# Optimization experiments

Hardware: AMD Instinct MI355X
Metric: run time of the kernel (lower is better)

## Reference

```python
import jax, jax.numpy as jnp
import numpy as np
from jax.ops import segment_sum

N_NODES = 100000


def _add_self_loops(edge_index, n):
    loop = jnp.arange(n, dtype=edge_index.dtype)
    src = jnp.concatenate([edge_index[0], loop])
    dst = jnp.concatenate([edge_index[1], loop])
    return src, dst


def _gcn_conv(x, W, b, src, dst, n):
    # PyG GCNConv: h = X W; out[i] = sum_j norm(j,i) h[j] + b, with self-loops
    h = x @ W                                             # [N, out]
    deg = segment_sum(jnp.ones_like(src, dtype=x.dtype), dst, num_segments=n)
    dinv = jnp.where(deg > 0, jax.lax.rsqrt(deg), 0.0)    # deg^{-1/2}
    norm = dinv[src] * dinv[dst]                          # [E]
    msg = h[src] * norm[:, None]                          # gather + scale
    out = segment_sum(msg, dst, num_segments=n)           # scatter-add
    return out + b


def setup_inputs() -> dict:
    key = jax.random.key(0)
    ks = jax.random.split(key, 8)
    x = jax.random.normal(ks[0], (N_NODES, 128), dtype=jnp.float32)
    edge_index = jax.random.randint(ks[1], (2, 600000), 0, N_NODES, dtype=jnp.int64)
    s1 = 1.0 / np.sqrt(128); s2 = 1.0 / np.sqrt(64); s3 = 1.0 / np.sqrt(32)
    return {
        "x": x,
        "edge_index": edge_index,
        "W1": jax.random.uniform(ks[2], (128, 64), jnp.float32, -s1, s1),
        "b1": jnp.zeros((64,), jnp.float32),
        "W2": jax.random.uniform(ks[3], (64, 32), jnp.float32, -s2, s2),
        "b2": jnp.zeros((32,), jnp.float32),
        "Wc": jax.random.uniform(ks[4], (32, 1), jnp.float32, -s3, s3),
        "bc": jnp.zeros((1,), jnp.float32),
    }


def reference(x, edge_index, W1, b1, W2, b2, Wc, bc):
    n = x.shape[0]
    src, dst = _add_self_loops(edge_index, n)
    h = jax.nn.relu(_gcn_conv(x, W1, b1, src, dst, n))
    h = jax.nn.relu(_gcn_conv(h, W2, b2, src, dst, n))
    return h @ Wc + bc
```

## Files before the change

kernel.cpp:

```cpp
#include <hip/hip_runtime.h>


#define SCAN_THREADS 256
#define SCAN_PER_T   8
#define SCAN_TILE    (SCAN_THREADS * SCAN_PER_T)

__global__ __launch_bounds__(256) void count_kernel(const int* __restrict__ dst,
                                                    int* __restrict__ deg, int E) {
    int e = blockIdx.x * blockDim.x + threadIdx.x;
    if (e < E) atomicAdd(&deg[dst[e]], 1);
}

__global__ __launch_bounds__(SCAN_THREADS) void tile_reduce_kernel(const int* __restrict__ deg,
                                                                   int* __restrict__ bsum,
                                                                   int n) {
    __shared__ int s[SCAN_THREADS];
    int t = threadIdx.x;
    int gbase = blockIdx.x * SCAN_TILE + t * SCAN_PER_T;
    int local = 0;
#pragma unroll
    for (int k = 0; k < SCAN_PER_T; ++k) {
        int i = gbase + k;
        if (i < n) local += deg[i];
    }
    s[t] = local;
    __syncthreads();
    for (int off = SCAN_THREADS / 2; off > 0; off >>= 1) {
        if (t < off) s[t] += s[t + off];
        __syncthreads();
    }
    if (t == 0) bsum[blockIdx.x] = s[0];
}

__global__ __launch_bounds__(SCAN_THREADS) void scan_bsums_kernel(int* __restrict__ bsum,
                                                                  int* __restrict__ row_ptr,
                                                                  int nb, int n) {
    __shared__ int s[SCAN_THREADS];
    int t = threadIdx.x;
    s[t] = (t < nb) ? bsum[t] : 0;
    __syncthreads();
    for (int off = 1; off < SCAN_THREADS; off <<= 1) {
        int v = (t >= off) ? s[t - off] : 0;
        __syncthreads();
        s[t] += v;
        __syncthreads();
    }
    if (t < nb) bsum[t] = (t == 0) ? 0 : s[t - 1];
    if (t == 0) row_ptr[n] = s[nb - 1];
}

__global__ __launch_bounds__(SCAN_THREADS) void tile_apply_kernel(int* __restrict__ deg,
                                                                  const int* __restrict__ bsum,
                                                                  int* __restrict__ row_ptr,
                                                                  float* __restrict__ dinv,
                                                                  int n) {
    __shared__ int s[SCAN_THREADS];
    int t = threadIdx.x;
    int gbase = blockIdx.x * SCAN_TILE + t * SCAN_PER_T;

    int d[SCAN_PER_T];
    int inc[SCAN_PER_T];
    int run = 0;
#pragma unroll
    for (int k = 0; k < SCAN_PER_T; ++k) {
        int i = gbase + k;
        d[k] = (i < n) ? deg[i] : 0;
        run += d[k];
        inc[k] = run;
    }
    s[t] = run;
    __syncthreads();
    for (int off = 1; off < SCAN_THREADS; off <<= 1) {
        int v = (t >= off) ? s[t - off] : 0;
        __syncthreads();
        s[t] += v;
        __syncthreads();
    }
    int base = bsum[blockIdx.x] + ((t == 0) ? 0 : s[t - 1]);
#pragma unroll
    for (int k = 0; k < SCAN_PER_T; ++k) {
        int i = gbase + k;
        if (i < n) {
            int ex = base + inc[k] - d[k];
            row_ptr[i] = ex;
            deg[i] = ex;
            dinv[i] = rsqrtf((float)(d[k] + 1));
        }
    }
}

__global__ __launch_bounds__(256) void fill_kernel(const int* __restrict__ src,
                                                   const int* __restrict__ dst,
                                                   int* __restrict__ cursor,
                                                   int* __restrict__ col, int E) {
    int e = blockIdx.x * blockDim.x + threadIdx.x;
    if (e < E) {
        int pos = atomicAdd(&cursor[dst[e]], 1);
        col[pos] = src[e];
    }
}

template <int IN, int OUT, int BM, int TM, int TN>
__global__ __launch_bounds__(256) void gemm_tiled(const float* __restrict__ X,
                                                  const float* __restrict__ W,
                                                  float* __restrict__ H, int n) {
    constexpr int BK = 32;
    constexpr int XST = BK + 1;
    constexpr int NTX = OUT / TN;
    constexpr int NF4 = BM * BK / 4;
    static_assert(NTX * (BM / TM) == 256, "thread mapping");

    __shared__ float Ws[IN * OUT];
    __shared__ float Xs[BM * XST];

    const int t = threadIdx.x;
    for (int i = t; i < IN * OUT / 4; i += 256)
        ((float4*)Ws)[i] = ((const float4*)W)[i];

    const int node0 = blockIdx.x * BM;
    const int tx = t % NTX;
    const int ty = t / NTX;
    const int row0 = ty * TM;
    const int jb = tx * TN;

    float acc[TM][TN];
#pragma unroll
    for (int i = 0; i < TM; ++i)
#pragma unroll
        for (int j = 0; j < TN; ++j) acc[i][j] = 0.f;

    for (int kt = 0; kt < IN / BK; ++kt) {
        __syncthreads();
        for (int f = t; f < NF4; f += 256) {
            int nd = f >> 3;
            int kq = f & 7;
            float4 val = make_float4(0.f, 0.f, 0.f, 0.f);
            if (node0 + nd < n)
                val = *(const float4*)(X + (size_t)(node0 + nd) * IN + kt * BK + kq * 4);
            float* p = Xs + nd * XST + kq * 4;
            p[0] = val.x; p[1] = val.y; p[2] = val.z; p[3] = val.w;
        }
        __syncthreads();

#pragma unroll 4
        for (int k = 0; k < BK; ++k) {
            float xv[TM];
#pragma unroll
            for (int i = 0; i < TM; ++i) xv[i] = Xs[(row0 + i) * XST + k];
            float4 wv = *(const float4*)(Ws + (size_t)(kt * BK + k) * OUT + jb);
#pragma unroll
            for (int i = 0; i < TM; ++i) {
                acc[i][0] += xv[i] * wv.x;
                acc[i][1] += xv[i] * wv.y;
                acc[i][2] += xv[i] * wv.z;
                acc[i][3] += xv[i] * wv.w;
            }
        }
    }

#pragma unroll
    for (int i = 0; i < TM; ++i) {
        int node = node0 + row0 + i;
        if (node < n)
            *(float4*)(H + (size_t)node * OUT + jb) =
                make_float4(acc[i][0], acc[i][1], acc[i][2], acc[i][3]);
    }
}

template <int F>
__global__ __launch_bounds__(256) void agg_relu_kernel(const int* __restrict__ row_ptr,
                                                       const int* __restrict__ col,
                                                       const float* __restrict__ dinv,
                                                       const float* __restrict__ H,
                                                       const float* __restrict__ b,
                                                       float* __restrict__ OUT, int n) {
    constexpr int TPE = F / 4;
    int t = blockIdx.x * blockDim.x + threadIdx.x;
    int node = t / TPE;
    int c = t % TPE;
    if (node >= n) return;
    int rs = row_ptr[node], re = row_ptr[node + 1];
    float di = dinv[node];
    float4 acc = make_float4(0.f, 0.f, 0.f, 0.f);
    int e = rs;
    for (; e + 1 < re; e += 2) {
        int s0 = col[e], s1 = col[e + 1];
        float w0 = dinv[s0], w1 = dinv[s1];
        float4 v0 = *(const float4*)(H + (size_t)s0 * F + c * 4);
        float4 v1 = *(const float4*)(H + (size_t)s1 * F + c * 4);
        acc.x += w0 * v0.x + w1 * v1.x;
        acc.y += w0 * v0.y + w1 * v1.y;
        acc.z += w0 * v0.z + w1 * v1.z;
        acc.w += w0 * v0.w + w1 * v1.w;
    }
    if (e < re) {
        int s0 = col[e];
        float w0 = dinv[s0];
        float4 v0 = *(const float4*)(H + (size_t)s0 * F + c * 4);
        acc.x += w0 * v0.x; acc.y += w0 * v0.y;
        acc.z += w0 * v0.z; acc.w += w0 * v0.w;
    }
    float4 hs = *(const float4*)(H + (size_t)node * F + c * 4);
    float4 bb = *(const float4*)(b + c * 4);
    float d2 = di * di;
    float4 r;
    r.x = di * acc.x + d2 * hs.x + bb.x;
    r.y = di * acc.y + d2 * hs.y + bb.y;
    r.z = di * acc.z + d2 * hs.z + bb.z;
    r.w = di * acc.w + d2 * hs.w + bb.w;
    r.x = r.x > 0.f ? r.x : 0.f;
    r.y = r.y > 0.f ? r.y : 0.f;
    r.z = r.z > 0.f ? r.z : 0.f;
    r.w = r.w > 0.f ? r.w : 0.f;
    *(float4*)(OUT + (size_t)node * F + c * 4) = r;
}

__global__ __launch_bounds__(256) void agg_final_kernel(const int* __restrict__ row_ptr,
                                                        const int* __restrict__ col,
                                                        const float* __restrict__ dinv,
                                                        const float* __restrict__ H,
                                                        const float* __restrict__ b2,
                                                        const float* __restrict__ Wc,
                                                        const float* __restrict__ bc,
                                                        float* __restrict__ out, int n) {
    constexpr int F = 32, TPE = 8;
    int t = blockIdx.x * blockDim.x + threadIdx.x;
    int node = t / TPE;
    int c = t % TPE;
    if (node >= n) return;
    int rs = row_ptr[node], re = row_ptr[node + 1];
    float di = dinv[node];
    float4 acc = make_float4(0.f, 0.f, 0.f, 0.f);
    int e = rs;
    for (; e + 1 < re; e += 2) {
        int s0 = col[e], s1 = col[e + 1];
        float w0 = dinv[s0], w1 = dinv[s1];
        float4 v0 = *(const float4*)(H + (size_t)s0 * F + c * 4);
        float4 v1 = *(const float4*)(H + (size_t)s1 * F + c * 4);
        acc.x += w0 * v0.x + w1 * v1.x;
        acc.y += w0 * v0.y + w1 * v1.y;
        acc.z += w0 * v0.z + w1 * v1.z;
        acc.w += w0 * v0.w + w1 * v1.w;
    }
    if (e < re) {
        int s0 = col[e];
        float w0 = dinv[s0];
        float4 v0 = *(const float4*)(H + (size_t)s0 * F + c * 4);
        acc.x += w0 * v0.x; acc.y += w0 * v0.y;
        acc.z += w0 * v0.z; acc.w += w0 * v0.w;
    }
    float4 hs = *(const float4*)(H + (size_t)node * F + c * 4);
    float4 bb = *(const float4*)(b2 + c * 4);
    float4 wc = *(const float4*)(Wc + c * 4);
    float d2 = di * di;
    float4 r;
    r.x = di * acc.x + d2 * hs.x + bb.x;
    r.y = di * acc.y + d2 * hs.y + bb.y;
    r.z = di * acc.z + d2 * hs.z + bb.z;
    r.w = di * acc.w + d2 * hs.w + bb.w;
    float dot = (r.x > 0.f ? r.x : 0.f) * wc.x + (r.y > 0.f ? r.y : 0.f) * wc.y +
                (r.z > 0.f ? r.z : 0.f) * wc.z + (r.w > 0.f ? r.w : 0.f) * wc.w;
    dot += __shfl_xor(dot, 1, 8);
    dot += __shfl_xor(dot, 2, 8);
    dot += __shfl_xor(dot, 4, 8);
    if (c == 0) out[node] = dot + bc[0];
}

extern "C" void kernel_launch(void* const* d_in, const int* in_sizes, int n_in,
                              void* d_out, int out_size, void* d_ws, size_t ws_size,
                              hipStream_t stream) {
    const float* x  = (const float*)d_in[0];
    const int*   ei = (const int*)d_in[1];
    const float* W1 = (const float*)d_in[2];
    const float* b1 = (const float*)d_in[3];
    const float* W2 = (const float*)d_in[4];
    const float* b2 = (const float*)d_in[5];
    const float* Wc = (const float*)d_in[6];
    const float* bc = (const float*)d_in[7];
    float* out = (float*)d_out;

    const int n = in_sizes[0] / 128;
    const int E = in_sizes[1] / 2;

    const int* src = ei;
    const int* dst = ei + (size_t)E;

    const int nb = (n + SCAN_TILE - 1) / SCAN_TILE;

    float* dinv    = (float*)d_ws;
    int*   deg     = (int*)d_ws + n;
    int*   row_ptr = (int*)d_ws + 2 * (size_t)n;
    int*   col     = row_ptr + (n + 1);
    int*   bsum    = col + E;
    float* bufA    = (float*)(bsum + 256);
    float* bufB    = bufA + (size_t)n * 64;

    hipMemsetAsync(deg, 0, (size_t)n * 4, stream);
    count_kernel<<<(E + 255) / 256, 256, 0, stream>>>(dst, deg, E);
    tile_reduce_kernel<<<nb, SCAN_THREADS, 0, stream>>>(deg, bsum, n);
    scan_bsums_kernel<<<1, SCAN_THREADS, 0, stream>>>(bsum, row_ptr, nb, n);
    tile_apply_kernel<<<nb, SCAN_THREADS, 0, stream>>>(deg, bsum, row_ptr, dinv, n);
    fill_kernel<<<(E + 255) / 256, 256, 0, stream>>>(src, dst, deg, col, E);

    const int gemm_grid = (n + 127) / 128;

    gemm_tiled<128, 64, 128, 8, 4><<<gemm_grid, 256, 0, stream>>>(x, W1, bufA, n);
    agg_relu_kernel<64><<<(n * 16 + 255) / 256, 256, 0, stream>>>(row_ptr, col, dinv,
                                                                  bufA, b1, bufB, n);
    gemm_tiled<64, 32, 128, 4, 4><<<gemm_grid, 256, 0, stream>>>(bufB, W2, bufA, n);
    agg_final_kernel<<<(n * 8 + 255) / 256, 256, 0, stream>>>(row_ptr, col, dinv,
                                                              bufA, b2, Wc, bc, out, n);
}
```

Before: 268.9 us.

## Double-buffer transposed X tile in GEMM with register-staged prefetch

The X tile in the tiled GEMM is now stored transposed (k-major with padded stride) in shared memory, so each thread reads its rows with a float4 load instead of scalar loads. The next K-slice is prefetched from global memory into registers while the current slice is computed, with two shared buffers alternating. This aims to hide global load latency and cut LDS instruction count. It assumes BM=128 (hardcoded 4x32 rows per stage), which ties the kernel to that template configuration, and it adds register pressure.

```diff
diff --git a/kernel.cpp b/kernel.cpp
--- a/kernel.cpp
+++ b/kernel.cpp
@@ -105,13 +105,13 @@
                                                   const float* __restrict__ W,
                                                   float* __restrict__ H, int n) {
     constexpr int BK = 32;
-    constexpr int XST = BK + 1;
+    constexpr int S = 132;
     constexpr int NTX = OUT / TN;
-    constexpr int NF4 = BM * BK / 4;
+    constexpr int NKT = IN / BK;
     static_assert(NTX * (BM / TM) == 256, "thread mapping");
 
     __shared__ float Ws[IN * OUT];
-    __shared__ float Xs[BM * XST];
+    __shared__ float Xs[2][BK * S];
 
     const int t = threadIdx.x;
     for (int i = t; i < IN * OUT / 4; i += 256)
@@ -123,31 +123,60 @@
     const int row0 = ty * TM;
     const int jb = tx * TN;
 
+    const int snd = t >> 3;
+    const int skq = t & 7;
+
     float acc[TM][TN];
 #pragma unroll
     for (int i = 0; i < TM; ++i)
 #pragma unroll
         for (int j = 0; j < TN; ++j) acc[i][j] = 0.f;
 
-    for (int kt = 0; kt < IN / BK; ++kt) {
-        __syncthreads();
-        for (int f = t; f < NF4; f += 256) {
-            int nd = f >> 3;
-            int kq = f & 7;
-            float4 val = make_float4(0.f, 0.f, 0.f, 0.f);
-            if (node0 + nd < n)
-                val = *(const float4*)(X + (size_t)(node0 + nd) * IN + kt * BK + kq * 4);
-            float* p = Xs + nd * XST + kq * 4;
-            p[0] = val.x; p[1] = val.y; p[2] = val.z; p[3] = val.w;
+    float4 stg[4];
+#pragma unroll
+    for (int i = 0; i < 4; ++i) {
+        int nd = snd + 32 * i;
+        stg[i] = make_float4(0.f, 0.f, 0.f, 0.f);
+        if (node0 + nd < n)
+            stg[i] = *(const float4*)(X + (size_t)(node0 + nd) * IN + skq * 4);
+    }
+
+    int cur = 0;
+    for (int kt = 0; kt < NKT; ++kt) {
+#pragma unroll
+        for (int i = 0; i < 4; ++i) {
+            int nd = snd + 32 * i;
+            float* p = Xs[cur] + (skq * 4) * S + nd;
+            p[0 * S] = stg[i].x;
+            p[1 * S] = stg[i].y;
+            p[2 * S] = stg[i].z;
+            p[3 * S] = stg[i].w;
         }
         __syncthreads();
 
+        if (kt + 1 < NKT) {
+#pragma unroll
+            for (int i = 0; i < 4; ++i) {
+                int nd = snd + 32 * i;
+                stg[i] = make_float4(0.f, 0.f, 0.f, 0.f);
+                if (node0 + nd < n)
+                    stg[i] = *(const float4*)(X + (size_t)(node0 + nd) * IN +
+                                              (kt + 1) * BK + skq * 4);
+            }
+        }
+
+        const float* xb = Xs[cur];
+        const float* wb = Ws + (size_t)kt * BK * OUT + jb;
 #pragma unroll 4
         for (int k = 0; k < BK; ++k) {
+            float4 wv = *(const float4*)(wb + (size_t)k * OUT);
             float xv[TM];
 #pragma unroll
-            for (int i = 0; i < TM; ++i) xv[i] = Xs[(row0 + i) * XST + k];
-            float4 wv = *(const float4*)(Ws + (size_t)(kt * BK + k) * OUT + jb);
+            for (int i4 = 0; i4 < TM; i4 += 4) {
+                float4 xq = *(const float4*)(xb + k * S + row0 + i4);
+                xv[i4 + 0] = xq.x; xv[i4 + 1] = xq.y;
+                xv[i4 + 2] = xq.z; xv[i4 + 3] = xq.w;
+            }
 #pragma unroll
             for (int i = 0; i < TM; ++i) {
                 acc[i][0] += xv[i] * wv.x;
@@ -156,6 +185,8 @@
                 acc[i][3] += xv[i] * wv.w;
             }
         }
+        __syncthreads();
+        cur ^= 1;
     }
 
 #pragma unroll
```

After: 267.0 us. No clear change (-0.7%).
